# Kernel tuning notes

Measured on AMD Instinct MI355X. Metric: run time of the kernel, lower is better.

The kernel has to match this reference:

```python
import jax, jax.numpy as jnp
import numpy as np

K = 3  # kernel size
PAD = 1
C_IN = 32
C_OUT = 32
CKK = C_IN * K * K  # 288
HID = C_OUT  # hidden width of kernel-generator MLP


def _unfold(x):
    """torch F.unfold equivalent, (C, kh, kw)-major. x: [B,C,H,W] -> [B, C*K*K, H*W]."""
    B, C, H, W = x.shape
    xp = jnp.pad(x, ((0, 0), (0, 0), (PAD, PAD), (PAD, PAD)))
    # stack K*K shifted views -> [B, C, K*K, H, W]
    patches = jnp.stack(
        [xp[:, :, i:i + H, j:j + W] for i in range(K) for j in range(K)], axis=2
    )
    return patches.reshape(B, C * K * K, H * W)


def setup_inputs() -> dict:
    key = jax.random.key(0)
    ks = jax.random.split(key, 6)
    B, H, W = 2, 64, 64
    x = jax.random.normal(ks[0], (B, C_IN, H, W), dtype=jnp.float32)
    # kernel_generator: Linear(CKK -> HID), Tanh, Linear(HID -> C_OUT*CKK)
    s1 = 1.0 / np.sqrt(CKK)
    s2 = 1.0 / np.sqrt(HID)
    W1 = jax.random.uniform(ks[1], (HID, CKK), jnp.float32, -s1, s1)
    b1 = jax.random.uniform(ks[2], (HID,), jnp.float32, -s1, s1)
    W2 = jax.random.uniform(ks[3], (C_OUT * CKK, HID), jnp.float32, -s2, s2)
    b2 = jax.random.uniform(ks[4], (C_OUT * CKK,), jnp.float32, -s2, s2)
    bias = jax.random.uniform(ks[5], (C_OUT,), jnp.float32, -s1, s1)
    return {"x": x, "W1": W1, "b1": b1, "W2": W2, "b2": b2, "bias": bias}


def reference(x, W1, b1, W2, b2, bias):
    B, C, H, W = x.shape
    L = H * W
    u = _unfold(x)                       # [B, CKK, L]
    ut = u.transpose(0, 2, 1)            # [B, L, CKK]
    h = jnp.tanh(jnp.einsum('blj,hj->blh', ut, W1) + b1)          # [B, L, HID]
    kern = jnp.einsum('blh,oh->blo', h, W2) + b2                  # [B, L, C_OUT*CKK]
    kern = kern.reshape(B, L, C_OUT, CKK)                         # per-pixel kernels
    out = jnp.einsum('bloj,blj->bol', kern, ut)                   # [B, C_OUT, L]
    out = out.reshape(B, C_OUT, H, W) + bias[None, :, None, None]
    return out
```

## Files before the change

### kernel.cpp

```cpp
#include <hip/hip_runtime.h>
#include <hip/hip_bf16.h>


#define CKK 288
#define SJ  296

typedef __attribute__((ext_vector_type(8))) short short8;
typedef __attribute__((ext_vector_type(4))) float f32x4;

#define W2F_OFF 0
#define W1B_OFF 294912
#define B2B_OFF (294912 + 9216)
#define WS_ELEMS (294912 + 9216 + 9216)

__global__ __launch_bounds__(256) void prep_kernel(
    const float* __restrict__ W1, const float* __restrict__ W2,
    const float* __restrict__ b2, __hip_bfloat16* __restrict__ ws)
{
    int s = blockIdx.x * 256 + threadIdx.x;
    if (s < 294912) {
        int o = s / 9216, rem = s - o * 9216;
        int j = rem >> 5, h = rem & 31;
        int w8 = o * 2 + (h >> 4);
        int kb = j >> 5;
        int l  = ((j >> 3) & 3) * 16 + (h & 15);
        int e  = j & 7;
        ws[W2F_OFF + (w8 * 9 + kb) * 512 + l * 8 + e] = __float2bfloat16(W2[s]);
    } else if (s < 294912 + 9216) {
        int k = s - 294912;
        ws[W1B_OFF + k] = __float2bfloat16(W1[k]);
    } else if (s < WS_ELEMS) {
        int k = s - (294912 + 9216);
        ws[B2B_OFF + k] = __float2bfloat16(b2[k]);
    }
}

__global__ __launch_bounds__(256, 4) void dynaconv_main(
    const float* __restrict__ x,
    const float* __restrict__ b1,
    const float* __restrict__ bias,
    const __hip_bfloat16* __restrict__ ws,
    float* __restrict__ out)
{
    __shared__ __hip_bfloat16 u_lds[32 * SJ];
    __shared__ float hh_lds[32 * 33];
    __shared__ float t_lds[32 * 8];
    __shared__ float o_stage[8][32];

    const int t  = threadIdx.x;
    const int w  = t >> 6;
    const int l  = t & 63;
    const int lg = l >> 4;
    const int lr = l & 15;

    const int nt = blockIdx.x & 3, mt = blockIdx.x >> 2;
    const int o0 = nt * 8;
    const int g0 = mt * 32;
    const int b  = g0 >> 12;
    const int l0 = g0 & 4095;
    const int y  = l0 >> 6;
    const int wx0 = l0 & 63;

    #pragma unroll
    for (int k = 0; k < 36; ++k) {
        int idx = k * 256 + t;
        int j = idx >> 5, p = idx & 31;
        int c = j / 9, r = j - c * 9;
        int ki = r / 3, kj = r - ki * 3;
        int y2 = y + ki - 1;
        int x2 = wx0 + p + kj - 1;
        float v = 0.f;
        if ((unsigned)y2 < 64u && (unsigned)x2 < 64u)
            v = x[((b * 32 + c) * 64 + y2) * 64 + x2];
        u_lds[p * SJ + j] = __float2bfloat16(v);
    }
    __syncthreads();

    if (w < 3) {
        const __hip_bfloat16* w1b = ws + W1B_OFF;
        const __hip_bfloat16* b2b = ws + B2B_OFF;
        f32x4 acc0 = {0.f,0.f,0.f,0.f}, acc1 = {0.f,0.f,0.f,0.f};
        #pragma unroll
        for (int kb = 0; kb < 9; ++kb) {
            short8 bf;
            if (w < 2)
                bf = *(const short8*)(w1b + (w * 16 + lr) * CKK + kb * 32 + lg * 8);
            else if (lr < 8)
                bf = *(const short8*)(b2b + (o0 + lr) * CKK + kb * 32 + lg * 8);
            else
                bf = short8{0,0,0,0,0,0,0,0};
            short8 a0 = *(const short8*)(u_lds + lr * SJ + kb * 32 + lg * 8);
            short8 a1 = *(const short8*)(u_lds + (16 + lr) * SJ + kb * 32 + lg * 8);
            acc0 = __builtin_amdgcn_mfma_f32_16x16x32_bf16(a0, bf, acc0, 0, 0, 0);
            acc1 = __builtin_amdgcn_mfma_f32_16x16x32_bf16(a1, bf, acc1, 0, 0, 0);
        }
        if (w < 2) {
            const int col = w * 16 + lr;
            float b1v = b1[col];
            #pragma unroll
            for (int r = 0; r < 4; ++r) {
                hh_lds[(lg * 4 + r) * 33 + col]      = tanhf(acc0[r] + b1v);
                hh_lds[(16 + lg * 4 + r) * 33 + col] = tanhf(acc1[r] + b1v);
            }
        } else if (lr < 8) {
            float bv = bias[o0 + lr];
            #pragma unroll
            for (int r = 0; r < 4; ++r) {
                t_lds[(lg * 4 + r) * 8 + lr]      = acc0[r] + bv;
                t_lds[(16 + lg * 4 + r) * 8 + lr] = acc1[r] + bv;
            }
        }
    }
    __syncthreads();

    f32x4 acc[2][4];
    #pragma unroll
    for (int m = 0; m < 2; ++m)
        #pragma unroll
        for (int nf = 0; nf < 4; ++nf)
            acc[m][nf] = f32x4{0.f, 0.f, 0.f, 0.f};

    {
        const __hip_bfloat16* W2f = ws + W2F_OFF;
        const int ckbase = (o0 * 2 + w * 4) * 9;
        short8 bcur[4];
        #pragma unroll
        for (int nf = 0; nf < 4; ++nf)
            bcur[nf] = *(const short8*)(W2f + (size_t)(ckbase + nf * 9) * 512 + l * 8);

        #pragma unroll
        for (int kb = 0; kb < 9; ++kb) {
            short8 a0 = *(const short8*)(u_lds + lr * SJ + kb * 32 + lg * 8);
            short8 a1 = *(const short8*)(u_lds + (16 + lr) * SJ + kb * 32 + lg * 8);
            short8 bnext[4];
            if (kb < 8) {
                #pragma unroll
                for (int nf = 0; nf < 4; ++nf)
                    bnext[nf] = *(const short8*)(W2f + (size_t)(ckbase + nf * 9 + kb + 1) * 512 + l * 8);
            }
            #pragma unroll
            for (int nf = 0; nf < 4; ++nf) {
                acc[0][nf] = __builtin_amdgcn_mfma_f32_16x16x32_bf16(a0, bcur[nf], acc[0][nf], 0, 0, 0);
                acc[1][nf] = __builtin_amdgcn_mfma_f32_16x16x32_bf16(a1, bcur[nf], acc[1][nf], 0, 0, 0);
            }
            if (kb < 8) {
                #pragma unroll
                for (int nf = 0; nf < 4; ++nf)
                    bcur[nf] = bnext[nf];
            }
        }
    }

    #pragma unroll
    for (int ol = 0; ol < 2; ++ol) {
        const int o_loc = w * 2 + ol;
        #pragma unroll
        for (int m = 0; m < 2; ++m) {
            #pragma unroll
            for (int r = 0; r < 4; ++r) {
                const int p = m * 16 + lg * 4 + r;
                float v = hh_lds[p * 33 + lr]      * acc[m][ol * 2][r]
                        + hh_lds[p * 33 + 16 + lr] * acc[m][ol * 2 + 1][r];
                v += __shfl_xor(v, 1);
                v += __shfl_xor(v, 2);
                v += __shfl_xor(v, 4);
                v += __shfl_xor(v, 8);
                if (lr == 0) o_stage[o_loc][p] = v;
            }
        }
    }
    __syncthreads();

    {
        int o_l = t >> 5, p = t & 31;
        float val = o_stage[o_l][p] + t_lds[p * 8 + o_l];
        out[((size_t)(b * 32 + o0 + o_l)) * 4096 + l0 + p] = val;
    }
}

extern "C" void kernel_launch(void* const* d_in, const int* in_sizes, int n_in,
                              void* d_out, int out_size, void* d_ws, size_t ws_size,
                              hipStream_t stream) {
    const float* x    = (const float*)d_in[0];
    const float* W1   = (const float*)d_in[1];
    const float* b1   = (const float*)d_in[2];
    const float* W2   = (const float*)d_in[3];
    const float* b2   = (const float*)d_in[4];
    const float* bias = (const float*)d_in[5];
    float* out = (float*)d_out;
    __hip_bfloat16* ws = (__hip_bfloat16*)d_ws;

    prep_kernel<<<(WS_ELEMS + 255) / 256, 256, 0, stream>>>(W1, W2, b2, ws);
    dynaconv_main<<<1024, 256, 0, stream>>>(x, b1, bias, ws, out);
}
```

Before: 30.93 us.

## Retile dynamic conv to full-row pixel tiles with four output channels per block

Each block now covers a full 64-pixel image row and 4 output channels instead of 32 pixels and 8 channels. The grid stays at 1024 blocks, but each wave now owns one output channel. The im2col gather is restructured so each thread loads one pixel for one channel and row at a time, which gives coalesced row reads of x. The unfolded tile is staged in LDS and reused across 4 M-fragments. The cost is doubled LDS use and lower occupancy (launch bounds 3), and the hidden-layer MLP is recomputed in every block for each group of 4 output channels, which doubles that redundant work.

```diff
diff --git a/kernel.cpp b/kernel.cpp
--- a/kernel.cpp
+++ b/kernel.cpp
@@ -35,17 +35,17 @@
     }
 }
 
-__global__ __launch_bounds__(256, 4) void dynaconv_main(
+__global__ __launch_bounds__(256, 3) void dynaconv_main(
     const float* __restrict__ x,
     const float* __restrict__ b1,
     const float* __restrict__ bias,
     const __hip_bfloat16* __restrict__ ws,
     float* __restrict__ out)
 {
-    __shared__ __hip_bfloat16 u_lds[32 * SJ];
-    __shared__ float hh_lds[32 * 33];
-    __shared__ float t_lds[32 * 8];
-    __shared__ float o_stage[8][32];
+    __shared__ __hip_bfloat16 u_lds[64 * SJ];
+    __shared__ float hh_lds[64 * 33];
+    __shared__ float t_lds[64 * 4];
+    __shared__ float o_stage[4][64];
 
     const int t  = threadIdx.x;
     const int w  = t >> 6;
@@ -53,128 +53,124 @@
     const int lg = l >> 4;
     const int lr = l & 15;
 
-    const int nt = blockIdx.x & 3, mt = blockIdx.x >> 2;
-    const int o0 = nt * 8;
-    const int g0 = mt * 32;
-    const int b  = g0 >> 12;
-    const int l0 = g0 & 4095;
-    const int y  = l0 >> 6;
-    const int wx0 = l0 & 63;
+    const int nt = blockIdx.x & 7;
+    const int mt = blockIdx.x >> 3;
+    const int o0 = nt * 4;
+    const int b  = mt >> 6;
+    const int y  = mt & 63;
+    const int o_w = o0 + w;
 
-    #pragma unroll
-    for (int k = 0; k < 36; ++k) {
-        int idx = k * 256 + t;
-        int j = idx >> 5, p = idx & 31;
-        int c = j / 9, r = j - c * 9;
-        int ki = r / 3, kj = r - ki * 3;
-        int y2 = y + ki - 1;
-        int x2 = wx0 + p + kj - 1;
-        float v = 0.f;
-        if ((unsigned)y2 < 64u && (unsigned)x2 < 64u)
-            v = x[((b * 32 + c) * 64 + y2) * 64 + x2];
-        u_lds[p * SJ + j] = __float2bfloat16(v);
-    }
-    __syncthreads();
-
-    if (w < 3) {
-        const __hip_bfloat16* w1b = ws + W1B_OFF;
-        const __hip_bfloat16* b2b = ws + B2B_OFF;
-        f32x4 acc0 = {0.f,0.f,0.f,0.f}, acc1 = {0.f,0.f,0.f,0.f};
+    for (int cc = 0; cc < 8; ++cc) {
+        const int c = w * 8 + cc;
+        const float* xc = x + ((size_t)(b * 32 + c)) * 4096;
         #pragma unroll
-        for (int kb = 0; kb < 9; ++kb) {
-            short8 bf;
-            if (w < 2)
-                bf = *(const short8*)(w1b + (w * 16 + lr) * CKK + kb * 32 + lg * 8);
-            else if (lr < 8)
-                bf = *(const short8*)(b2b + (o0 + lr) * CKK + kb * 32 + lg * 8);
-            else
-                bf = short8{0,0,0,0,0,0,0,0};
-            short8 a0 = *(const short8*)(u_lds + lr * SJ + kb * 32 + lg * 8);
-            short8 a1 = *(const short8*)(u_lds + (16 + lr) * SJ + kb * 32 + lg * 8);
-            acc0 = __builtin_amdgcn_mfma_f32_16x16x32_bf16(a0, bf, acc0, 0, 0, 0);
-            acc1 = __builtin_amdgcn_mfma_f32_16x16x32_bf16(a1, bf, acc1, 0, 0, 0);
-        }
-        if (w < 2) {
-            const int col = w * 16 + lr;
-            float b1v = b1[col];
-            #pragma unroll
-            for (int r = 0; r < 4; ++r) {
-                hh_lds[(lg * 4 + r) * 33 + col]      = tanhf(acc0[r] + b1v);
-                hh_lds[(16 + lg * 4 + r) * 33 + col] = tanhf(acc1[r] + b1v);
-            }
-        } else if (lr < 8) {
-            float bv = bias[o0 + lr];
-            #pragma unroll
-            for (int r = 0; r < 4; ++r) {
-                t_lds[(lg * 4 + r) * 8 + lr]      = acc0[r] + bv;
-                t_lds[(16 + lg * 4 + r) * 8 + lr] = acc1[r] + bv;
+        for (int ki = 0; ki < 3; ++ki) {
+            const int y2 = y + ki - 1;
+            const int jb = c * 9 + ki * 3;
+            if ((unsigned)y2 < 64u) {
+                const float* xr = xc + y2 * 64;
+                #pragma unroll
+                for (int kj = 0; kj < 3; ++kj) {
+                    int x2 = l + kj - 1;
+                    float v = ((unsigned)x2 < 64u) ? xr[x2] : 0.f;
+                    u_lds[l * SJ + jb + kj] = __float2bfloat16(v);
+                }
+            } else {
+                #pragma unroll
+                for (int kj = 0; kj < 3; ++kj)
+                    u_lds[l * SJ + jb + kj] = __float2bfloat16(0.f);
             }
         }
     }
     __syncthreads();
 
-    f32x4 acc[2][4];
+    if (w < 3) {
+        f32x4 acc[4];
+        #pragma unroll
+        for (int mf = 0; mf < 4; ++mf) acc[mf] = f32x4{0.f,0.f,0.f,0.f};
+        const __hip_bfloat16* Bmat = ws + ((w < 2) ? W1B_OFF : B2B_OFF);
+        const int col = (w < 2) ? (w * 16 + lr) : (o0 + lr);
+        const bool valid = (w < 2) || (lr < 4);
+        #pragma unroll
+        for (int kb = 0; kb < 9; ++kb) {
+            short8 bf = valid ? *(const short8*)(Bmat + col * CKK + kb * 32 + lg * 8)
+                              : short8{0,0,0,0,0,0,0,0};
+            #pragma unroll
+            for (int mf = 0; mf < 4; ++mf) {
+                short8 a = *(const short8*)(u_lds + (mf * 16 + lr) * SJ + kb * 32 + lg * 8);
+                acc[mf] = __builtin_amdgcn_mfma_f32_16x16x32_bf16(a, bf, acc[mf], 0, 0, 0);
+            }
+        }
+        if (w < 2) {
+            float b1v = b1[col];
+            #pragma unroll
+            for (int mf = 0; mf < 4; ++mf)
+                #pragma unroll
+                for (int r = 0; r < 4; ++r)
+                    hh_lds[(mf * 16 + lg * 4 + r) * 33 + col] = tanhf(acc[mf][r] + b1v);
+        } else if (lr < 4) {
+            float bv = bias[o0 + lr];
+            #pragma unroll
+            for (int mf = 0; mf < 4; ++mf)
+                #pragma unroll
+                for (int r = 0; r < 4; ++r)
+                    t_lds[(mf * 16 + lg * 4 + r) * 4 + lr] = acc[mf][r] + bv;
+        }
+    }
+    __syncthreads();
+
+    f32x4 acc[4][2];
     #pragma unroll
-    for (int m = 0; m < 2; ++m)
-        #pragma unroll
-        for (int nf = 0; nf < 4; ++nf)
-            acc[m][nf] = f32x4{0.f, 0.f, 0.f, 0.f};
-
+    for (int mf = 0; mf < 4; ++mf) {
+        acc[mf][0] = f32x4{0.f,0.f,0.f,0.f};
+        acc[mf][1] = f32x4{0.f,0.f,0.f,0.f};
+    }
     {
         const __hip_bfloat16* W2f = ws + W2F_OFF;
-        const int ckbase = (o0 * 2 + w * 4) * 9;
-        short8 bcur[4];
+        const int ckbase = o_w * 18;
+        short8 bcur[2];
         #pragma unroll
-        for (int nf = 0; nf < 4; ++nf)
+        for (int nf = 0; nf < 2; ++nf)
             bcur[nf] = *(const short8*)(W2f + (size_t)(ckbase + nf * 9) * 512 + l * 8);
 
         #pragma unroll
         for (int kb = 0; kb < 9; ++kb) {
-            short8 a0 = *(const short8*)(u_lds + lr * SJ + kb * 32 + lg * 8);
-            short8 a1 = *(const short8*)(u_lds + (16 + lr) * SJ + kb * 32 + lg * 8);
-            short8 bnext[4];
+            short8 bnext[2];
             if (kb < 8) {
                 #pragma unroll
-                for (int nf = 0; nf < 4; ++nf)
+                for (int nf = 0; nf < 2; ++nf)
                     bnext[nf] = *(const short8*)(W2f + (size_t)(ckbase + nf * 9 + kb + 1) * 512 + l * 8);
             }
             #pragma unroll
-            for (int nf = 0; nf < 4; ++nf) {
-                acc[0][nf] = __builtin_amdgcn_mfma_f32_16x16x32_bf16(a0, bcur[nf], acc[0][nf], 0, 0, 0);
-                acc[1][nf] = __builtin_amdgcn_mfma_f32_16x16x32_bf16(a1, bcur[nf], acc[1][nf], 0, 0, 0);
+            for (int mf = 0; mf < 4; ++mf) {
+                short8 a = *(const short8*)(u_lds + (mf * 16 + lr) * SJ + kb * 32 + lg * 8);
+                acc[mf][0] = __builtin_amdgcn_mfma_f32_16x16x32_bf16(a, bcur[0], acc[mf][0], 0, 0, 0);
+                acc[mf][1] = __builtin_amdgcn_mfma_f32_16x16x32_bf16(a, bcur[1], acc[mf][1], 0, 0, 0);
             }
-            if (kb < 8) {
-                #pragma unroll
-                for (int nf = 0; nf < 4; ++nf)
-                    bcur[nf] = bnext[nf];
-            }
+            if (kb < 8) { bcur[0] = bnext[0]; bcur[1] = bnext[1]; }
         }
     }
 
     #pragma unroll
-    for (int ol = 0; ol < 2; ++ol) {
-        const int o_loc = w * 2 + ol;
+    for (int mf = 0; mf < 4; ++mf) {
         #pragma unroll
-        for (int m = 0; m < 2; ++m) {
-            #pragma unroll
-            for (int r = 0; r < 4; ++r) {
-                const int p = m * 16 + lg * 4 + r;
-                float v = hh_lds[p * 33 + lr]      * acc[m][ol * 2][r]
-                        + hh_lds[p * 33 + 16 + lr] * acc[m][ol * 2 + 1][r];
-                v += __shfl_xor(v, 1);
-                v += __shfl_xor(v, 2);
-                v += __shfl_xor(v, 4);
-                v += __shfl_xor(v, 8);
-                if (lr == 0) o_stage[o_loc][p] = v;
-            }
+        for (int r = 0; r < 4; ++r) {
+            const int p = mf * 16 + lg * 4 + r;
+            float v = hh_lds[p * 33 + lr]      * acc[mf][0][r]
+                    + hh_lds[p * 33 + 16 + lr] * acc[mf][1][r];
+            v += __shfl_xor(v, 1);
+            v += __shfl_xor(v, 2);
+            v += __shfl_xor(v, 4);
+            v += __shfl_xor(v, 8);
+            if (lr == 0) o_stage[w][p] = v;
         }
     }
     __syncthreads();
 
     {
-        int o_l = t >> 5, p = t & 31;
-        float val = o_stage[o_l][p] + t_lds[p * 8 + o_l];
-        out[((size_t)(b * 32 + o0 + o_l)) * 4096 + l0 + p] = val;
+        const int o_l = t >> 6, p = t & 63;
+        float val = o_stage[o_l][p] + t_lds[p * 4 + o_l];
+        out[((size_t)(b * 32 + o0 + o_l)) * 4096 + y * 64 + p] = val;
     }
 }
 
```

Result: slower. 40.18 us (+29.9%).
